# Optimization experiments

Measured on AMD Instinct MI355X. Metric: run time of the kernel, lower is better.

Reference implementation:

```python
import math
import jax, jax.numpy as jnp
import numpy as np

N_STEPS = 4

def rotate_half(x):
    h = x.shape[-1] // 2
    return jnp.concatenate([-x[..., h:], x[..., :h]], axis=-1)

def setup_inputs() -> dict:
    key = jax.random.key(0)
    k0, k1, k2, k3 = jax.random.split(key, 4)
    B, N, F, D = 2, 4096, 512, 64
    features = jax.random.normal(k0, (B, N, F), jnp.float32)
    # standard RoPE tables, shape [N, D]
    inv_freq = 1.0 / (10000.0 ** (jnp.arange(0, D, 2, dtype=jnp.float32) / D))
    ang = jnp.arange(N, dtype=jnp.float32)[:, None] * inv_freq[None, :]  # [N, D/2]
    ang = jnp.concatenate([ang, ang], axis=-1)  # [N, D]
    cos, sin = jnp.cos(ang), jnp.sin(ang)
    # causal mask broadcast to [B, N, N]
    mask = jnp.broadcast_to(jnp.tril(jnp.ones((N, N), bool)), (B, N, N))
    s = 1.0 / math.sqrt(F)
    Wq = jax.random.normal(k1, (F, D), jnp.float32) * s
    Wk = jax.random.normal(k2, (F, D), jnp.float32) * s
    charge_w = jax.random.normal(k3, (F, 1), jnp.float32) * s
    charge_b = jnp.zeros((1,), jnp.float32)
    step_size = jnp.full((1,), 0.5, jnp.float32)
    charge_decay = jnp.full((1,), 0.3, jnp.float32)
    return dict(features=features, cos=cos, sin=sin, mask=mask, Wq=Wq, Wk=Wk,
                charge_w=charge_w, charge_b=charge_b,
                step_size=step_size, charge_decay=charge_decay)

def reference(features, cos, sin, mask, Wq, Wk, charge_w, charge_b, step_size, charge_decay):
    d_k = Wq.shape[-1]
    Q = jnp.einsum('bnf,fd->bnd', features, Wq)
    K = jnp.einsum('bnf,fd->bnd', features, Wk)
    c, s = cos[None, :, :], sin[None, :, :]  # broadcast over batch
    Q = Q * c + rotate_half(Q) * s
    K = K * c + rotate_half(K) * s
    compat = jnp.einsum('bnd,bmd->bnm', Q, K) / math.sqrt(d_k)  # [B,N,N]
    charge = jax.nn.sigmoid(jnp.einsum('bnf,fo->bno', features, charge_w)[..., 0] + charge_b[0])  # [B,N]
    neg_inf = jnp.asarray(-jnp.inf, compat.dtype)
    logits = jnp.where(mask, compat, neg_inf)
    ss = step_size[0]
    cd = charge_decay[0]
    for _ in range(N_STEPS):
        attn = jax.nn.softmax(logits, axis=-1)
        received = attn.sum(axis=-2)  # column sums, [B,N]
        charge = charge * (1.0 - cd * jax.nn.sigmoid(received - 1.0))
        energy = -compat * charge[..., :, None] * charge[..., None, :]
        logits = jnp.where(mask, logits - ss * energy, neg_inf)
    return jax.nn.softmax(logits, axis=-1)
```

## Files before the change

kernel.cpp:

```cpp
#include <hip/hip_runtime.h>
#include <math.h>

#define NTOK   4096
#define NFEAT  512
#define NDIM   64
#define RROWS  8
#define NBANDS (NTOK / RROWS)

__device__ __forceinline__ float block_max256(float v, float* s) {
#pragma unroll
  for (int o = 32; o > 0; o >>= 1) v = fmaxf(v, __shfl_down(v, o, 64));
  int tid = threadIdx.x;
  if ((tid & 63) == 0) s[tid >> 6] = v;
  __syncthreads();
  v = fmaxf(fmaxf(s[0], s[1]), fmaxf(s[2], s[3]));
  __syncthreads();
  return v;
}
__device__ __forceinline__ float block_sum256(float v, float* s) {
#pragma unroll
  for (int o = 32; o > 0; o >>= 1) v += __shfl_down(v, o, 64);
  int tid = threadIdx.x;
  if ((tid & 63) == 0) s[tid >> 6] = v;
  __syncthreads();
  v = s[0] + s[1] + s[2] + s[3];
  __syncthreads();
  return v;
}

__global__ __launch_bounds__(256) void qk_kernel(
    const float* __restrict__ feat, const float* __restrict__ cosb,
    const float* __restrict__ sinb, const float* __restrict__ Wq,
    const float* __restrict__ Wk, const float* __restrict__ cw,
    const float* __restrict__ cbp, float* __restrict__ Q, float* __restrict__ K,
    float* __restrict__ cur, float* __restrict__ chist)
{
  __shared__ __align__(16) float smem[RROWS * NFEAT];
  const int tid  = threadIdx.x;
  const int row0 = blockIdx.x * RROWS;

  const float4* fb4 = (const float4*)(feat + (size_t)row0 * NFEAT);
  float4* sm4 = (float4*)smem;
#pragma unroll
  for (int i = tid; i < RROWS * NFEAT / 4; i += 256) sm4[i] = fb4[i];
  if (tid < RROWS * 4) chist[row0 * 4 + tid] = 0.f;
  __syncthreads();

  const int r   = tid >> 5;
  const int c   = tid & 31;
  const int isQ = (c < 16);
  const int d0  = (c & 15) * 4;
  const float* __restrict__ Wp = isQ ? Wq : Wk;
  const float* fr = smem + (r << 9);

  float a0 = 0.f, a1 = 0.f, a2 = 0.f, a3 = 0.f;
  for (int k = 0; k < NFEAT; ++k) {
    float fv = fr[k];
    float4 w = *(const float4*)(Wp + k * NDIM + d0);
    a0 = fmaf(fv, w.x, a0); a1 = fmaf(fv, w.y, a1);
    a2 = fmaf(fv, w.z, a2); a3 = fmaf(fv, w.w, a3);
  }

  float accc = 0.f;
#pragma unroll
  for (int j = 0; j < 16; ++j) accc = fmaf(fr[c + (j << 5)], cw[c + (j << 5)], accc);
#pragma unroll
  for (int o = 16; o > 0; o >>= 1) accc += __shfl_down(accc, o, 64);
  if (c == 0) {
    float cb = cbp[0];
    cur[row0 + r] = 1.f / (1.f + __expf(-(accc + cb)));
  }
  __syncthreads();

  float* sraw = smem;
  {
    float* dst = sraw + r * 132 + (isQ ? 0 : 64) + d0;
    dst[0] = a0; dst[1] = a1; dst[2] = a2; dst[3] = a3;
  }
  __syncthreads();

#pragma unroll
  for (int i = tid; i < RROWS * NDIM; i += 256) {
    int rr = i >> 6, d = i & 63;
    int g = row0 + rr, n = g & (NTOK - 1);
    float cv = cosb[(n << 6) + d], sv = sinb[(n << 6) + d];
    float qv = sraw[rr * 132 + d];
    float qr = (d < 32) ? -sraw[rr * 132 + d + 32] : sraw[rr * 132 + d - 32];
    Q[(size_t)g * NDIM + d] = qv * cv + qr * sv;
    float kv = sraw[rr * 132 + 64 + d];
    float kr = (d < 32) ? -sraw[rr * 132 + 64 + d + 32] : sraw[rr * 132 + 64 + d - 32];
    K[(size_t)g * NDIM + d] = kv * cv + kr * sv;
  }
}

__global__ __launch_bounds__(256) void compat_kernel(
    const float* __restrict__ Q, const float* __restrict__ K, float* __restrict__ C)
{
  __shared__ __align__(16) float Qs[32][132];
  __shared__ __align__(16) float Ks[32][132];
  int p = blockIdx.x, b = 0;
  if (p >= 528) { b = 1; p -= 528; }
  int ti = (int)((sqrtf(8.f * p + 1.f) - 1.f) * 0.5f);
  while ((ti + 1) * (ti + 2) / 2 <= p) ++ti;
  while (ti * (ti + 1) / 2 > p) --ti;
  int tj = p - ti * (ti + 1) / 2;

  const int tid = threadIdx.x;
  const int ty = tid >> 4, tx = tid & 15;
  const int i0 = ty * 8, j0 = tx * 8;
  const size_t qbase = ((size_t)b * NTOK + (size_t)ti * 128) * NDIM;
  const size_t kbase = ((size_t)b * NTOK + (size_t)tj * 128) * NDIM;

  float acc[8][8];
#pragma unroll
  for (int ii = 0; ii < 8; ++ii)
#pragma unroll
    for (int jj = 0; jj < 8; ++jj) acc[ii][jj] = 0.f;

  for (int dk = 0; dk < NDIM; dk += 32) {
    __syncthreads();
    for (int i = tid; i < 128 * 32; i += 256) {
      int row = i >> 5, d = i & 31;
      Qs[d][row] = Q[qbase + (size_t)row * NDIM + dk + d];
      Ks[d][row] = K[kbase + (size_t)row * NDIM + dk + d];
    }
    __syncthreads();
#pragma unroll
    for (int d = 0; d < 32; ++d) {
      float4 q0 = *(const float4*)&Qs[d][i0];
      float4 q1 = *(const float4*)&Qs[d][i0 + 4];
      float4 k0 = *(const float4*)&Ks[d][j0];
      float4 k1 = *(const float4*)&Ks[d][j0 + 4];
      float av[8] = {q0.x, q0.y, q0.z, q0.w, q1.x, q1.y, q1.z, q1.w};
      float bv[8] = {k0.x, k0.y, k0.z, k0.w, k1.x, k1.y, k1.z, k1.w};
#pragma unroll
      for (int ii = 0; ii < 8; ++ii)
#pragma unroll
        for (int jj = 0; jj < 8; ++jj)
          acc[ii][jj] = fmaf(av[ii], bv[jj], acc[ii][jj]);
    }
  }
#pragma unroll
  for (int ii = 0; ii < 8; ++ii) {
    size_t grow = (size_t)b * NTOK + (size_t)ti * 128 + i0 + ii;
    float4 w0 = make_float4(acc[ii][0] * 0.125f, acc[ii][1] * 0.125f,
                            acc[ii][2] * 0.125f, acc[ii][3] * 0.125f);
    float4 w1 = make_float4(acc[ii][4] * 0.125f, acc[ii][5] * 0.125f,
                            acc[ii][6] * 0.125f, acc[ii][7] * 0.125f);
    *(float4*)&C[grow * NTOK + (size_t)tj * 128 + j0]     = w0;
    *(float4*)&C[grow * NTOK + (size_t)tj * 128 + j0 + 4] = w1;
  }
}

template <int MODE>
__global__ __launch_bounds__(256) void pass_kernel(
    const float* __restrict__ compat, const float4* __restrict__ chist,
    const float* __restrict__ ssp, float* __restrict__ partial,
    float* __restrict__ out)
{
  __shared__ float sred[4];
  const int tid = threadIdx.x;
  int band = blockIdx.x, b = 0;
  if (band >= NBANDS) { b = 1; band -= NBANDS; }
  const int n0 = band * RROWS;
  const int kmax = (n0 + RROWS - 1) >> 8;
  const float ss = ssp[0];

  float4 ch[16];
#pragma unroll
  for (int k = 0; k < 16; ++k)
    if (k <= kmax) ch[k] = chist[(b << 12) + tid + (k << 8)];

  float cs[16];
#pragma unroll
  for (int k = 0; k < 16; ++k) cs[k] = 0.f;

  for (int rr = 0; rr < RROWS; ++rr) {
    const int n = n0 + rr;
    const float* rowp = compat + ((size_t)((b << 12) + n) << 12);
    float4 h = chist[(b << 12) + n];
    h.x *= ss; h.y *= ss; h.z *= ss; h.w *= ss;

    float e[16];
    float vmax = -INFINITY;
#pragma unroll
    for (int k = 0; k < 16; ++k) {
      if (k > kmax) continue;
      const int col = tid + (k << 8);
      float x = -INFINITY;
      if (col <= n) {
        float cv  = rowp[col];
        float dot = fmaf(ch[k].x, h.x,
                    fmaf(ch[k].y, h.y, fmaf(ch[k].z, h.z, ch[k].w * h.w)));
        x = fmaf(cv, dot, cv);
      }
      e[k] = x;
      vmax = fmaxf(vmax, x);
    }
    float M = block_max256(vmax, sred);
    float lsum = 0.f;
#pragma unroll
    for (int k = 0; k < 16; ++k) {
      if (k > kmax) continue;
      float v = __expf(e[k] - M);
      e[k] = v;
      lsum += v;
    }
    float L = block_sum256(lsum, sred);
    float inv = 1.f / L;
    if (MODE == 0) {
#pragma unroll
      for (int k = 0; k < 16; ++k)
        if (k <= kmax) cs[k] += e[k] * inv;
    } else {
      float* orow = out + ((size_t)((b << 12) + n) << 12);
#pragma unroll
      for (int k = 0; k < 16; ++k) {
        if (k <= kmax) orow[tid + (k << 8)] = e[k] * inv;
        else           orow[tid + (k << 8)] = 0.f;
      }
    }
  }
  if (MODE == 0) {
    float* pp = partial + ((size_t)b * NBANDS + band) * NTOK;
    const int cmax = n0 + RROWS - 1;
#pragma unroll
    for (int k = 0; k < 16; ++k) {
      if (k > kmax) continue;
      int col = tid + (k << 8);
      if (col <= cmax) pp[col] = cs[k];
    }
  }
}

__global__ __launch_bounds__(256) void reduce_update_kernel(
    const float* __restrict__ partial, const float* __restrict__ cdp,
    float* __restrict__ cur, float* __restrict__ chist, int step)
{
  __shared__ float s[8][32];
  const int tid = threadIdx.x;
  const int b = blockIdx.x >> 7;
  const int m0 = (blockIdx.x & 127) << 5;
  const int ml = tid & 31, seg = tid >> 5;
  const int m = m0 + ml;
  const int bmin = m >> 3;
  float sum = 0.f;
  const float* pb = partial + (size_t)b * NBANDS * NTOK + m;
  for (int band = bmin + seg; band < NBANDS; band += 8)
    sum += pb[(size_t)band << 12];
  s[seg][ml] = sum;
  __syncthreads();
  if (seg == 0) {
    float r = s[0][ml] + s[1][ml] + s[2][ml] + s[3][ml] +
              s[4][ml] + s[5][ml] + s[6][ml] + s[7][ml];
    float sg = 1.f / (1.f + __expf(-(r - 1.f)));
    float cd = cdp[0];
    int idx = (b << 12) + m;
    float c = cur[idx] * (1.f - cd * sg);
    cur[idx] = c;
    chist[idx * 4 + step] = c;
  }
}

extern "C" void kernel_launch(void* const* d_in, const int* in_sizes, int n_in,
                              void* d_out, int out_size, void* d_ws, size_t ws_size,
                              hipStream_t stream) {
  const float* feat = (const float*)d_in[0];
  const float* cosb = (const float*)d_in[1];
  const float* sinb = (const float*)d_in[2];
  const float* Wq  = (const float*)d_in[4];
  const float* Wk  = (const float*)d_in[5];
  const float* cw  = (const float*)d_in[6];
  const float* cbp = (const float*)d_in[7];
  const float* ssp = (const float*)d_in[8];
  const float* cdp = (const float*)d_in[9];
  float* out = (float*)d_out;

  float* ws      = (float*)d_ws;
  float* Q       = ws;
  float* K       = ws + 524288;
  float* chist   = ws + 1048576;
  float* cur     = ws + 1081344;
  float* partial = ws + 1089536;

  qk_kernel<<<1024, 256, 0, stream>>>(feat, cosb, sinb, Wq, Wk, cw, cbp, Q, K, cur, chist);
  compat_kernel<<<1056, 256, 0, stream>>>(Q, K, out);
  for (int t = 0; t < 4; ++t) {
    pass_kernel<0><<<2 * NBANDS, 256, 0, stream>>>(out, (const float4*)chist, ssp, partial, nullptr);
    reduce_update_kernel<<<256, 256, 0, stream>>>(partial, cdp, cur, chist, t);
  }
  pass_kernel<1><<<2 * NBANDS, 256, 0, stream>>>(out, (const float4*)chist, ssp, nullptr, out);
}
```

Baseline: 732.8 us.

## Fuse iterative softmax passes into one persistent kernel with grid barriers

Replaces the nine pass and reduce launches with a single persistent kernel of 512 blocks. Each block handles two mirrored causal bands to balance triangular work, and the blocks synchronise through atomic global barriers between the sweep and fold phases. Rows are now read with float4 loads, the per-step charge history is stored per step with compile-time step counts, and the old chist zeroing is removed. This cuts launch overhead and balances load, but relies on all 512 blocks being co-resident, which risks deadlock if occupancy is lower.

```diff
diff --git a/kernel.cpp b/kernel.cpp
--- a/kernel.cpp
+++ b/kernel.cpp
@@ -4,8 +4,7 @@
 #define NTOK   4096
 #define NFEAT  512
 #define NDIM   64
-#define RROWS  8
-#define NBANDS (NTOK / RROWS)
+#define NBLK   512
 
 __device__ __forceinline__ float block_max256(float v, float* s) {
 #pragma unroll
@@ -33,17 +32,16 @@
     const float* __restrict__ sinb, const float* __restrict__ Wq,
     const float* __restrict__ Wk, const float* __restrict__ cw,
     const float* __restrict__ cbp, float* __restrict__ Q, float* __restrict__ K,
-    float* __restrict__ cur, float* __restrict__ chist)
+    float* __restrict__ cur)
 {
-  __shared__ __align__(16) float smem[RROWS * NFEAT];
+  __shared__ __align__(16) float smem[8 * NFEAT];
   const int tid  = threadIdx.x;
-  const int row0 = blockIdx.x * RROWS;
+  const int row0 = blockIdx.x * 8;
 
   const float4* fb4 = (const float4*)(feat + (size_t)row0 * NFEAT);
   float4* sm4 = (float4*)smem;
 #pragma unroll
-  for (int i = tid; i < RROWS * NFEAT / 4; i += 256) sm4[i] = fb4[i];
-  if (tid < RROWS * 4) chist[row0 * 4 + tid] = 0.f;
+  for (int i = tid; i < 8 * NFEAT / 4; i += 256) sm4[i] = fb4[i];
   __syncthreads();
 
   const int r   = tid >> 5;
@@ -80,7 +78,7 @@
   __syncthreads();
 
 #pragma unroll
-  for (int i = tid; i < RROWS * NDIM; i += 256) {
+  for (int i = tid; i < 8 * NDIM; i += 256) {
     int rr = i >> 6, d = i & 63;
     int g = row0 + rr, n = g & (NTOK - 1);
     float cv = cosb[(n << 6) + d], sv = sinb[(n << 6) + d];
@@ -152,114 +150,182 @@
   }
 }
 
-template <int MODE>
-__global__ __launch_bounds__(256) void pass_kernel(
-    const float* __restrict__ compat, const float4* __restrict__ chist,
-    const float* __restrict__ ssp, float* __restrict__ partial,
-    float* __restrict__ out)
-{
-  __shared__ float sred[4];
-  const int tid = threadIdx.x;
-  int band = blockIdx.x, b = 0;
-  if (band >= NBANDS) { b = 1; band -= NBANDS; }
-  const int n0 = band * RROWS;
-  const int kmax = (n0 + RROWS - 1) >> 8;
-  const float ss = ssp[0];
-
-  float4 ch[16];
-#pragma unroll
-  for (int k = 0; k < 16; ++k)
-    if (k <= kmax) ch[k] = chist[(b << 12) + tid + (k << 8)];
-
-  float cs[16];
-#pragma unroll
-  for (int k = 0; k < 16; ++k) cs[k] = 0.f;
-
-  for (int rr = 0; rr < RROWS; ++rr) {
+__global__ void init_bars(int* bars) {
+  if (threadIdx.x < 64) bars[threadIdx.x] = 0;
+}
+
+__device__ __forceinline__ void gbar(int* bars, int slot) {
+  __syncthreads();
+  if (threadIdx.x == 0) {
+    __threadfence();
+    __hip_atomic_fetch_add(&bars[slot], 1, __ATOMIC_RELEASE, __HIP_MEMORY_SCOPE_AGENT);
+    while (__hip_atomic_load(&bars[slot], __ATOMIC_ACQUIRE, __HIP_MEMORY_SCOPE_AGENT) < NBLK)
+      __builtin_amdgcn_s_sleep(8);
+    __threadfence();
+  }
+  __syncthreads();
+}
+
+template <int T, bool FINAL>
+__device__ void sweep_unit(int u, float* CC, const float* cstep, float ss,
+                           float* partial, float* sred) {
+  const int tid  = threadIdx.x;
+  const int b    = u >> 9, band = u & 511;
+  const int n0   = band << 3;
+  const int cb   = tid << 2;
+  float* base = CC + ((size_t)((b << 12) + n0) << 12);
+
+  float4 ct[T ? T : 1][4];
+#pragma unroll
+  for (int t2 = 0; t2 < T; ++t2)
+#pragma unroll
+    for (int q = 0; q < 4; ++q)
+      ct[t2][q] = *(const float4*)(cstep + t2 * 2 * NTOK + (b << 12) + cb + (q << 10));
+
+  float4 cs[4];
+#pragma unroll
+  for (int q = 0; q < 4; ++q) cs[q] = make_float4(0.f, 0.f, 0.f, 0.f);
+
+  for (int rr = 0; rr < 8; ++rr) {
     const int n = n0 + rr;
-    const float* rowp = compat + ((size_t)((b << 12) + n) << 12);
-    float4 h = chist[(b << 12) + n];
-    h.x *= ss; h.y *= ss; h.z *= ss; h.w *= ss;
-
-    float e[16];
+    float* rowp = base + ((size_t)rr << 12);
+    float hs[T ? T : 1];
+#pragma unroll
+    for (int t2 = 0; t2 < T; ++t2) hs[t2] = ss * cstep[t2 * 2 * NTOK + (b << 12) + n];
+
+    float4 e[4];
     float vmax = -INFINITY;
 #pragma unroll
-    for (int k = 0; k < 16; ++k) {
-      if (k > kmax) continue;
-      const int col = tid + (k << 8);
-      float x = -INFINITY;
-      if (col <= n) {
-        float cv  = rowp[col];
-        float dot = fmaf(ch[k].x, h.x,
-                    fmaf(ch[k].y, h.y, fmaf(ch[k].z, h.z, ch[k].w * h.w)));
-        x = fmaf(cv, dot, cv);
+    for (int q = 0; q < 4; ++q) {
+      const int c = cb + (q << 10);
+      if (c <= n) {
+        float4 cv = *(const float4*)(rowp + c);
+        float f0 = 1.f, f1 = 1.f, f2 = 1.f, f3 = 1.f;
+#pragma unroll
+        for (int t2 = 0; t2 < T; ++t2) {
+          f0 = fmaf(ct[t2][q].x, hs[t2], f0);
+          f1 = fmaf(ct[t2][q].y, hs[t2], f1);
+          f2 = fmaf(ct[t2][q].z, hs[t2], f2);
+          f3 = fmaf(ct[t2][q].w, hs[t2], f3);
+        }
+        e[q].x = cv.x * f0;
+        e[q].y = (c + 1 <= n) ? cv.y * f1 : -INFINITY;
+        e[q].z = (c + 2 <= n) ? cv.z * f2 : -INFINITY;
+        e[q].w = (c + 3 <= n) ? cv.w * f3 : -INFINITY;
+        vmax = fmaxf(vmax, fmaxf(fmaxf(e[q].x, e[q].y), fmaxf(e[q].z, e[q].w)));
+      } else {
+        e[q] = make_float4(-INFINITY, -INFINITY, -INFINITY, -INFINITY);
       }
-      e[k] = x;
-      vmax = fmaxf(vmax, x);
     }
     float M = block_max256(vmax, sred);
     float lsum = 0.f;
 #pragma unroll
-    for (int k = 0; k < 16; ++k) {
-      if (k > kmax) continue;
-      float v = __expf(e[k] - M);
-      e[k] = v;
-      lsum += v;
+    for (int q = 0; q < 4; ++q) {
+      e[q].x = __expf(e[q].x - M); e[q].y = __expf(e[q].y - M);
+      e[q].z = __expf(e[q].z - M); e[q].w = __expf(e[q].w - M);
+      lsum += (e[q].x + e[q].y) + (e[q].z + e[q].w);
     }
     float L = block_sum256(lsum, sred);
     float inv = 1.f / L;
-    if (MODE == 0) {
-#pragma unroll
-      for (int k = 0; k < 16; ++k)
-        if (k <= kmax) cs[k] += e[k] * inv;
+    if (FINAL) {
+#pragma unroll
+      for (int q = 0; q < 4; ++q) {
+        float4 w = make_float4(e[q].x * inv, e[q].y * inv, e[q].z * inv, e[q].w * inv);
+        *(float4*)(rowp + cb + (q << 10)) = w;
+      }
     } else {
-      float* orow = out + ((size_t)((b << 12) + n) << 12);
-#pragma unroll
-      for (int k = 0; k < 16; ++k) {
-        if (k <= kmax) orow[tid + (k << 8)] = e[k] * inv;
-        else           orow[tid + (k << 8)] = 0.f;
+#pragma unroll
+      for (int q = 0; q < 4; ++q) {
+        cs[q].x = fmaf(e[q].x, inv, cs[q].x);
+        cs[q].y = fmaf(e[q].y, inv, cs[q].y);
+        cs[q].z = fmaf(e[q].z, inv, cs[q].z);
+        cs[q].w = fmaf(e[q].w, inv, cs[q].w);
       }
     }
   }
-  if (MODE == 0) {
-    float* pp = partial + ((size_t)b * NBANDS + band) * NTOK;
-    const int cmax = n0 + RROWS - 1;
-#pragma unroll
-    for (int k = 0; k < 16; ++k) {
-      if (k > kmax) continue;
-      int col = tid + (k << 8);
-      if (col <= cmax) pp[col] = cs[k];
-    }
-  }
-}
-
-__global__ __launch_bounds__(256) void reduce_update_kernel(
-    const float* __restrict__ partial, const float* __restrict__ cdp,
-    float* __restrict__ cur, float* __restrict__ chist, int step)
-{
-  __shared__ float s[8][32];
+  if (!FINAL) {
+    float* pp = partial + ((size_t)(b * NBLK + band) << 12);
+    const int cmax = n0 + 7;
+#pragma unroll
+    for (int q = 0; q < 4; ++q) {
+      const int c = cb + (q << 10);
+      if (c + 3 <= cmax) {
+        *(float4*)(pp + c) = cs[q];
+      } else if (c <= cmax) {
+        pp[c] = cs[q].x;
+        if (c + 1 <= cmax) pp[c + 1] = cs[q].y;
+        if (c + 2 <= cmax) pp[c + 2] = cs[q].z;
+      }
+    }
+  }
+}
+
+__device__ void fold_unit(int bid, const float* partial, const float* cdp,
+                          float* cur, float* cstep, int step, float (*s)[16]) {
   const int tid = threadIdx.x;
-  const int b = blockIdx.x >> 7;
-  const int m0 = (blockIdx.x & 127) << 5;
-  const int ml = tid & 31, seg = tid >> 5;
-  const int m = m0 + ml;
+  const int lc = tid & 15, seg = tid >> 4;
+  const int g = (lc < 8) ? bid : (1023 - bid);
+  const int b = g >> 9;
+  const int m = ((g & 511) << 3) + (lc & 7);
   const int bmin = m >> 3;
   float sum = 0.f;
-  const float* pb = partial + (size_t)b * NBANDS * NTOK + m;
-  for (int band = bmin + seg; band < NBANDS; band += 8)
+  const float* pb = partial + (((size_t)b * NBLK) << 12) + m;
+  for (int band = bmin + seg; band < NBLK; band += 16)
     sum += pb[(size_t)band << 12];
-  s[seg][ml] = sum;
-  __syncthreads();
-  if (seg == 0) {
-    float r = s[0][ml] + s[1][ml] + s[2][ml] + s[3][ml] +
-              s[4][ml] + s[5][ml] + s[6][ml] + s[7][ml];
-    float sg = 1.f / (1.f + __expf(-(r - 1.f)));
-    float cd = cdp[0];
-    int idx = (b << 12) + m;
-    float c = cur[idx] * (1.f - cd * sg);
+  s[seg][lc] = sum;
+  __syncthreads();
+  if (tid < 16) {
+    const int lc2 = tid;
+    const int g2 = (lc2 < 8) ? bid : (1023 - bid);
+    const int b2 = g2 >> 9;
+    const int m2 = ((g2 & 511) << 3) + (lc2 & 7);
+    float r = 0.f;
+#pragma unroll
+    for (int sg = 0; sg < 16; ++sg) r += s[sg][lc2];
+    float sig = 1.f / (1.f + __expf(-(r - 1.f)));
+    const int idx = (b2 << 12) + m2;
+    float c = cur[idx] * (1.f - cdp[0] * sig);
     cur[idx] = c;
-    chist[idx * 4 + step] = c;
-  }
+    cstep[step * 2 * NTOK + idx] = c;
+  }
+  __syncthreads();
+}
+
+__global__ __launch_bounds__(256, 2) void fused_kernel(
+    float* CC, const float* __restrict__ ssp, const float* __restrict__ cdp,
+    float* cur, float* cstep, float* partial, int* bars) {
+  __shared__ float sred[4];
+  __shared__ float s[16][16];
+  const int bid = blockIdx.x;
+  const int u1 = bid, u2 = 1023 - bid;
+  const float ss = ssp[0];
+
+  sweep_unit<0, false>(u1, CC, cstep, ss, partial, sred);
+  sweep_unit<0, false>(u2, CC, cstep, ss, partial, sred);
+  gbar(bars, 0);
+  fold_unit(bid, partial, cdp, cur, cstep, 0, s);
+  gbar(bars, 1);
+
+  sweep_unit<1, false>(u1, CC, cstep, ss, partial, sred);
+  sweep_unit<1, false>(u2, CC, cstep, ss, partial, sred);
+  gbar(bars, 2);
+  fold_unit(bid, partial, cdp, cur, cstep, 1, s);
+  gbar(bars, 3);
+
+  sweep_unit<2, false>(u1, CC, cstep, ss, partial, sred);
+  sweep_unit<2, false>(u2, CC, cstep, ss, partial, sred);
+  gbar(bars, 4);
+  fold_unit(bid, partial, cdp, cur, cstep, 2, s);
+  gbar(bars, 5);
+
+  sweep_unit<3, false>(u1, CC, cstep, ss, partial, sred);
+  sweep_unit<3, false>(u2, CC, cstep, ss, partial, sred);
+  gbar(bars, 6);
+  fold_unit(bid, partial, cdp, cur, cstep, 3, s);
+  gbar(bars, 7);
+
+  sweep_unit<4, true>(u1, CC, cstep, ss, partial, sred);
+  sweep_unit<4, true>(u2, CC, cstep, ss, partial, sred);
 }
 
 extern "C" void kernel_launch(void* const* d_in, const int* in_sizes, int n_in,
@@ -279,15 +345,13 @@
   float* ws      = (float*)d_ws;
   float* Q       = ws;
   float* K       = ws + 524288;
-  float* chist   = ws + 1048576;
-  float* cur     = ws + 1081344;
+  float* cur     = ws + 1048576;
+  float* cstep   = ws + 1056768;
   float* partial = ws + 1089536;
-
-  qk_kernel<<<1024, 256, 0, stream>>>(feat, cosb, sinb, Wq, Wk, cw, cbp, Q, K, cur, chist);
+  int*   bars    = (int*)(ws + 5283840);
+
+  init_bars<<<1, 64, 0, stream>>>(bars);
+  qk_kernel<<<1024, 256, 0, stream>>>(feat, cosb, sinb, Wq, Wk, cw, cbp, Q, K, cur);
   compat_kernel<<<1056, 256, 0, stream>>>(Q, K, out);
-  for (int t = 0; t < 4; ++t) {
-    pass_kernel<0><<<2 * NBANDS, 256, 0, stream>>>(out, (const float4*)chist, ssp, partial, nullptr);
-    reduce_update_kernel<<<256, 256, 0, stream>>>(partial, cdp, cur, chist, t);
-  }
-  pass_kernel<1><<<2 * NBANDS, 256, 0, stream>>>(out, (const float4*)chist, ssp, nullptr, out);
-}
+  fused_kernel<<<NBLK, 256, 0, stream>>>(out, ssp, cdp, cur, cstep, partial, bars);
+}
```

After: 1.125 ms. 53.5% more time.

## Replace band softmax passes with wave-per-row sweeps and step-templated charge planes

Applied to the files above, without the earlier changes.

Each softmax row is now handled by a single 64-lane wave, using float4 loads and a shuffle-only reduction instead of block-wide syncthreads reductions. The max subtraction is dropped, since logits are bounded by scaled compat values, and the step count is a template parameter so the loops over past charges unroll. Rows are paired as p and 1023-p to balance causal work across blocks. Column sums are accumulated with LDS atomics per block and then folded by a smaller reduce kernel. The risks are LDS atomic contention and possible overflow in the unshifted exp.

```diff
diff --git a/kernel.cpp b/kernel.cpp
--- a/kernel.cpp
+++ b/kernel.cpp
@@ -4,46 +4,22 @@
 #define NTOK   4096
 #define NFEAT  512
 #define NDIM   64
-#define RROWS  8
-#define NBANDS (NTOK / RROWS)
-
-__device__ __forceinline__ float block_max256(float v, float* s) {
-#pragma unroll
-  for (int o = 32; o > 0; o >>= 1) v = fmaxf(v, __shfl_down(v, o, 64));
-  int tid = threadIdx.x;
-  if ((tid & 63) == 0) s[tid >> 6] = v;
-  __syncthreads();
-  v = fmaxf(fmaxf(s[0], s[1]), fmaxf(s[2], s[3]));
-  __syncthreads();
-  return v;
-}
-__device__ __forceinline__ float block_sum256(float v, float* s) {
-#pragma unroll
-  for (int o = 32; o > 0; o >>= 1) v += __shfl_down(v, o, 64);
-  int tid = threadIdx.x;
-  if ((tid & 63) == 0) s[tid >> 6] = v;
-  __syncthreads();
-  v = s[0] + s[1] + s[2] + s[3];
-  __syncthreads();
-  return v;
-}
 
 __global__ __launch_bounds__(256) void qk_kernel(
     const float* __restrict__ feat, const float* __restrict__ cosb,
     const float* __restrict__ sinb, const float* __restrict__ Wq,
     const float* __restrict__ Wk, const float* __restrict__ cw,
     const float* __restrict__ cbp, float* __restrict__ Q, float* __restrict__ K,
-    float* __restrict__ cur, float* __restrict__ chist)
-{
-  __shared__ __align__(16) float smem[RROWS * NFEAT];
+    float* __restrict__ cur)
+{
+  __shared__ __align__(16) float smem[8 * NFEAT];
   const int tid  = threadIdx.x;
-  const int row0 = blockIdx.x * RROWS;
+  const int row0 = blockIdx.x * 8;
 
   const float4* fb4 = (const float4*)(feat + (size_t)row0 * NFEAT);
   float4* sm4 = (float4*)smem;
 #pragma unroll
-  for (int i = tid; i < RROWS * NFEAT / 4; i += 256) sm4[i] = fb4[i];
-  if (tid < RROWS * 4) chist[row0 * 4 + tid] = 0.f;
+  for (int i = tid; i < 8 * NFEAT / 4; i += 256) sm4[i] = fb4[i];
   __syncthreads();
 
   const int r   = tid >> 5;
@@ -80,7 +56,7 @@
   __syncthreads();
 
 #pragma unroll
-  for (int i = tid; i < RROWS * NDIM; i += 256) {
+  for (int i = tid; i < 8 * NDIM; i += 256) {
     int rr = i >> 6, d = i & 63;
     int g = row0 + rr, n = g & (NTOK - 1);
     float cv = cosb[(n << 6) + d], sv = sinb[(n << 6) + d];
@@ -152,113 +128,120 @@
   }
 }
 
-template <int MODE>
-__global__ __launch_bounds__(256) void pass_kernel(
-    const float* __restrict__ compat, const float4* __restrict__ chist,
-    const float* __restrict__ ssp, float* __restrict__ partial,
-    float* __restrict__ out)
-{
-  __shared__ float sred[4];
-  const int tid = threadIdx.x;
-  int band = blockIdx.x, b = 0;
-  if (band >= NBANDS) { b = 1; band -= NBANDS; }
-  const int n0 = band * RROWS;
-  const int kmax = (n0 + RROWS - 1) >> 8;
+template <int T, bool FINAL>
+__global__ __launch_bounds__(256) void sweep_kernel(
+    float* __restrict__ CC, const float* __restrict__ cstep,
+    const float* __restrict__ ssp, float* __restrict__ partial)
+{
+  __shared__ float cs[NTOK];
+  const int tid  = threadIdx.x;
+  const int lane = tid & 63;
+  const int w    = tid >> 6;
+  const int bid  = blockIdx.x;
+  const int b    = bid >> 9;
+  const int p    = bid & 511;
   const float ss = ssp[0];
 
-  float4 ch[16];
-#pragma unroll
-  for (int k = 0; k < 16; ++k)
-    if (k <= kmax) ch[k] = chist[(b << 12) + tid + (k << 8)];
-
-  float cs[16];
-#pragma unroll
-  for (int k = 0; k < 16; ++k) cs[k] = 0.f;
-
-  for (int rr = 0; rr < RROWS; ++rr) {
-    const int n = n0 + rr;
-    const float* rowp = compat + ((size_t)((b << 12) + n) << 12);
-    float4 h = chist[(b << 12) + n];
-    h.x *= ss; h.y *= ss; h.z *= ss; h.w *= ss;
-
-    float e[16];
-    float vmax = -INFINITY;
+  if (!FINAL) {
+    for (int i = tid; i < NTOK; i += 256) cs[i] = 0.f;
+    __syncthreads();
+  }
+
+  float* base = CC + ((size_t)b << 24);
+  const float* planes = cstep + (b << 12);
+
+  const int rows[2] = { (p << 2) + w, ((1023 - p) << 2) + w };
+
+#pragma unroll
+  for (int ri = 0; ri < 2; ++ri) {
+    const int n = rows[ri];
+    const int kmax = n >> 8;
+    float* rowp = base + ((size_t)n << 12);
+
+    float hs[T ? T : 1];
+#pragma unroll
+    for (int t = 0; t < T; ++t) hs[t] = ss * planes[t * 2 * NTOK + n];
+
+    float4 e[16];
+    float lsum = 0.f;
 #pragma unroll
     for (int k = 0; k < 16; ++k) {
       if (k > kmax) continue;
-      const int col = tid + (k << 8);
-      float x = -INFINITY;
-      if (col <= n) {
-        float cv  = rowp[col];
-        float dot = fmaf(ch[k].x, h.x,
-                    fmaf(ch[k].y, h.y, fmaf(ch[k].z, h.z, ch[k].w * h.w)));
-        x = fmaf(cv, dot, cv);
+      const int c = (k << 8) + (lane << 2);
+      float4 cv = *(const float4*)(rowp + c);
+      float f0 = 1.f, f1 = 1.f, f2 = 1.f, f3 = 1.f;
+#pragma unroll
+      for (int t = 0; t < T; ++t) {
+        float4 ct = *(const float4*)(planes + t * 2 * NTOK + c);
+        f0 = fmaf(ct.x, hs[t], f0); f1 = fmaf(ct.y, hs[t], f1);
+        f2 = fmaf(ct.z, hs[t], f2); f3 = fmaf(ct.w, hs[t], f3);
       }
-      e[k] = x;
-      vmax = fmaxf(vmax, x);
-    }
-    float M = block_max256(vmax, sred);
-    float lsum = 0.f;
-#pragma unroll
-    for (int k = 0; k < 16; ++k) {
-      if (k > kmax) continue;
-      float v = __expf(e[k] - M);
-      e[k] = v;
-      lsum += v;
-    }
-    float L = block_sum256(lsum, sred);
-    float inv = 1.f / L;
-    if (MODE == 0) {
-#pragma unroll
-      for (int k = 0; k < 16; ++k)
-        if (k <= kmax) cs[k] += e[k] * inv;
+      float x0 = __expf(cv.x * f0);
+      float x1 = __expf(cv.y * f1);
+      float x2 = __expf(cv.z * f2);
+      float x3 = __expf(cv.w * f3);
+      e[k].x = (c     <= n) ? x0 : 0.f;
+      e[k].y = (c + 1 <= n) ? x1 : 0.f;
+      e[k].z = (c + 2 <= n) ? x2 : 0.f;
+      e[k].w = (c + 3 <= n) ? x3 : 0.f;
+      lsum += (e[k].x + e[k].y) + (e[k].z + e[k].w);
+    }
+#pragma unroll
+    for (int o = 1; o < 64; o <<= 1) lsum += __shfl_xor(lsum, o, 64);
+    const float inv = 1.f / lsum;
+
+    if (FINAL) {
+#pragma unroll
+      for (int k = 0; k < 16; ++k) {
+        const int c = (k << 8) + (lane << 2);
+        float4 wv = make_float4(0.f, 0.f, 0.f, 0.f);
+        if (k <= kmax)
+          wv = make_float4(e[k].x * inv, e[k].y * inv, e[k].z * inv, e[k].w * inv);
+        *(float4*)(rowp + c) = wv;
+      }
     } else {
-      float* orow = out + ((size_t)((b << 12) + n) << 12);
 #pragma unroll
       for (int k = 0; k < 16; ++k) {
-        if (k <= kmax) orow[tid + (k << 8)] = e[k] * inv;
-        else           orow[tid + (k << 8)] = 0.f;
+        if (k > kmax) continue;
+        const int c = (k << 8) + (lane << 2);
+        atomicAdd(&cs[c],     e[k].x * inv);
+        atomicAdd(&cs[c + 1], e[k].y * inv);
+        atomicAdd(&cs[c + 2], e[k].z * inv);
+        atomicAdd(&cs[c + 3], e[k].w * inv);
       }
     }
   }
-  if (MODE == 0) {
-    float* pp = partial + ((size_t)b * NBANDS + band) * NTOK;
-    const int cmax = n0 + RROWS - 1;
-#pragma unroll
-    for (int k = 0; k < 16; ++k) {
-      if (k > kmax) continue;
-      int col = tid + (k << 8);
-      if (col <= cmax) pp[col] = cs[k];
-    }
-  }
-}
-
-__global__ __launch_bounds__(256) void reduce_update_kernel(
+
+  if (!FINAL) {
+    __syncthreads();
+    const int len4 = (NTOK - 4 * p) >> 2;
+    float4* pp = (float4*)(partial + ((size_t)bid << 12));
+    const float4* cs4 = (const float4*)cs;
+    for (int i = tid; i < len4; i += 256) pp[i] = cs4[i];
+  }
+}
+
+__global__ __launch_bounds__(256) void fold_kernel(
     const float* __restrict__ partial, const float* __restrict__ cdp,
-    float* __restrict__ cur, float* __restrict__ chist, int step)
-{
-  __shared__ float s[8][32];
+    float* __restrict__ cur, float* __restrict__ cstep, int step)
+{
+  __shared__ float s[4][64];
   const int tid = threadIdx.x;
-  const int b = blockIdx.x >> 7;
-  const int m0 = (blockIdx.x & 127) << 5;
-  const int ml = tid & 31, seg = tid >> 5;
-  const int m = m0 + ml;
-  const int bmin = m >> 3;
-  float sum = 0.f;
-  const float* pb = partial + (size_t)b * NBANDS * NTOK + m;
-  for (int band = bmin + seg; band < NBANDS; band += 8)
-    sum += pb[(size_t)band << 12];
-  s[seg][ml] = sum;
+  const int ml = tid & 63, seg = tid >> 6;
+  const int idx = blockIdx.x * 64 + ml;
+  const int b = idx >> 12, m = idx & (NTOK - 1);
+  const int count = min(512, ((NTOK - 1 - m) >> 2) + 1);
+  const float* pp = partial + (((size_t)b << 9) << 12) + m;
+  float r = 0.f;
+  for (int q = seg; q < count; q += 4) r += pp[(size_t)q << 12];
+  s[seg][ml] = r;
   __syncthreads();
   if (seg == 0) {
-    float r = s[0][ml] + s[1][ml] + s[2][ml] + s[3][ml] +
-              s[4][ml] + s[5][ml] + s[6][ml] + s[7][ml];
-    float sg = 1.f / (1.f + __expf(-(r - 1.f)));
-    float cd = cdp[0];
-    int idx = (b << 12) + m;
-    float c = cur[idx] * (1.f - cd * sg);
+    float rr = s[0][ml] + s[1][ml] + s[2][ml] + s[3][ml];
+    float sig = 1.f / (1.f + __expf(-(rr - 1.f)));
+    float c = cur[idx] * (1.f - cdp[0] * sig);
     cur[idx] = c;
-    chist[idx * 4 + step] = c;
+    cstep[step * 2 * NTOK + idx] = c;
   }
 }
 
@@ -279,15 +262,20 @@
   float* ws      = (float*)d_ws;
   float* Q       = ws;
   float* K       = ws + 524288;
-  float* chist   = ws + 1048576;
-  float* cur     = ws + 1081344;
+  float* cur     = ws + 1048576;
+  float* cstep   = ws + 1056768;
   float* partial = ws + 1089536;
 
-  qk_kernel<<<1024, 256, 0, stream>>>(feat, cosb, sinb, Wq, Wk, cw, cbp, Q, K, cur, chist);
+  qk_kernel<<<1024, 256, 0, stream>>>(feat, cosb, sinb, Wq, Wk, cw, cbp, Q, K, cur);
   compat_kernel<<<1056, 256, 0, stream>>>(Q, K, out);
-  for (int t = 0; t < 4; ++t) {
-    pass_kernel<0><<<2 * NBANDS, 256, 0, stream>>>(out, (const float4*)chist, ssp, partial, nullptr);
-    reduce_update_kernel<<<256, 256, 0, stream>>>(partial, cdp, cur, chist, t);
-  }
-  pass_kernel<1><<<2 * NBANDS, 256, 0, stream>>>(out, (const float4*)chist, ssp, nullptr, out);
-}
+
+  sweep_kernel<0, false><<<1024, 256, 0, stream>>>(out, cstep, ssp, partial);
+  fold_kernel<<<128, 256, 0, stream>>>(partial, cdp, cur, cstep, 0);
+  sweep_kernel<1, false><<<1024, 256, 0, stream>>>(out, cstep, ssp, partial);
+  fold_kernel<<<128, 256, 0, stream>>>(partial, cdp, cur, cstep, 1);
+  sweep_kernel<2, false><<<1024, 256, 0, stream>>>(out, cstep, ssp, partial);
+  fold_kernel<<<128, 256, 0, stream>>>(partial, cdp, cur, cstep, 2);
+  sweep_kernel<3, false><<<1024, 256, 0, stream>>>(out, cstep, ssp, partial);
+  fold_kernel<<<128, 256, 0, stream>>>(partial, cdp, cur, cstep, 3);
+  sweep_kernel<4, true><<<1024, 256, 0, stream>>>(out, cstep, ssp, nullptr);
+}
```

Result: slower. 842.7 us (+15.0%).
